# Kernel optimization log

Measured on AMD Instinct MI355X. Metric: run time of the kernel, lower is better.

The kernel has to match this reference:

```python
import jax, jax.numpy as jnp
import numpy as np

# geomloss SamplesLoss('sinkhorn', blur=0.5, scaling=0.9, reach=None) defaults: p=2, debias=True
P = 2
BLUR = 0.5
SCALING = 0.9


def _sqdist_half(a, b):
    # C(x,y) = |x-y|^2 / 2  (geomloss p=2 cost), shape [N, M]
    a2 = jnp.sum(a * a, axis=1)
    b2 = jnp.sum(b * b, axis=1)
    return 0.5 * (a2[:, None] + b2[None, :]) - a @ b.T


def _softmin(eps, C, h):
    # softmin_tensorized: -eps * logsumexp_j( h_j - C_ij / eps ),  h = log-weights + dual/eps
    return -eps * jax.nn.logsumexp(h[None, :] - C / eps, axis=1)


def _eps_schedule(x, y):
    # geomloss epsilon_schedule: anneal eps from diameter^p down to blur^p by scaling^p
    xn, yn = np.asarray(x), np.asarray(y)
    mins = np.minimum(xn.min(axis=0), yn.min(axis=0))
    maxs = np.maximum(xn.max(axis=0), yn.max(axis=0))
    diameter = float(np.linalg.norm(maxs - mins))
    eps_list = [diameter ** P]
    eps_list += [float(np.exp(e)) for e in
                 np.arange(P * np.log(diameter), P * np.log(BLUR), P * np.log(SCALING))]
    eps_list += [BLUR ** P]
    return eps_list


def _sinkhorn_divergence(x, y, eps_list):
    N, M = x.shape[0], y.shape[0]
    C_xy = _sqdist_half(x, y)
    C_yx = C_xy.T
    C_xx = _sqdist_half(x, x)
    C_yy = _sqdist_half(y, y)
    a_log = jnp.full((N,), -float(np.log(N)), dtype=x.dtype)  # uniform weights, log domain
    b_log = jnp.full((M,), -float(np.log(M)), dtype=x.dtype)

    sg = jax.lax.stop_gradient
    Cxy_d, Cyx_d = sg(C_xy), sg(C_yx)
    Cxx_d, Cyy_d = sg(C_xx), sg(C_yy)

    # init at largest eps (= diameter^p)
    eps0 = eps_list[0]
    f_ba = _softmin(eps0, Cxy_d, b_log)
    g_ab = _softmin(eps0, Cyx_d, a_log)
    f_aa = _softmin(eps0, Cxx_d, a_log)
    g_bb = _softmin(eps0, Cyy_d, b_log)

    # symmetric (averaged) Sinkhorn updates along the eps-scaling schedule (no grad, like geomloss)
    for eps in eps_list:
        ft_ba = _softmin(eps, Cxy_d, b_log + g_ab / eps)
        gt_ab = _softmin(eps, Cyx_d, a_log + f_ba / eps)
        ft_aa = _softmin(eps, Cxx_d, a_log + f_aa / eps)
        gt_bb = _softmin(eps, Cyy_d, b_log + g_bb / eps)
        f_ba, g_ab = 0.5 * (f_ba + ft_ba), 0.5 * (g_ab + gt_ab)
        f_aa, g_bb = 0.5 * (f_aa + ft_aa), 0.5 * (g_bb + gt_bb)

    # last extrapolation at eps = blur^p; gradient flows only through the cost matrices here
    eps = eps_list[-1]
    f_ba, g_ab = (_softmin(eps, C_xy, sg(b_log + g_ab / eps)),
                  _softmin(eps, C_yx, sg(a_log + f_ba / eps)))
    f_aa = _softmin(eps, C_xx, sg(a_log + f_aa / eps))
    g_bb = _softmin(eps, C_yy, sg(b_log + g_bb / eps))

    # debiased divergence: <alpha, f_ba - f_aa> + <beta, g_ab - g_bb> (uniform weights -> mean)
    return jnp.mean(f_ba - f_aa) + jnp.mean(g_ab - g_bb)


def setup_inputs() -> dict:
    key = jax.random.key(0)
    kx, ky = jax.random.split(key)
    x = jax.random.normal(kx, (4096, 32), dtype=jnp.float32)
    y = jax.random.normal(ky, (4096, 32), dtype=jnp.float32)
    return {"x": x, "y": y}


def reference(x, y):
    eps_list = _eps_schedule(x, y)  # data-dependent schedule computed eagerly (as geomloss does)
    return _sinkhorn_divergence(x, y, eps_list)
```

## Files before the change

kernel.cpp:

```cpp
#include <hip/hip_runtime.h>
#include <math.h>

#define NPTS 4096
#define DIM  32
#define MAXSLOTS 52
#define NTHREADS 256
#define ITHREADS 512
#define NELEM 131072

#define WS_N2X   0
#define WS_N2Y   4096
#define WS_PMIN  8192
#define WS_PMAX  10240
#define WS_EPS   12288
#define WS_MODE  12352
#define WS_DUAL  12416
#define DUALSZ   16384
#define WS_BF    45184

#define M_SKIP   0
#define M_INIT   1
#define M_AVG    2
#define M_ASSIGN 3

typedef short   short8 __attribute__((ext_vector_type(8)));
typedef _Float16 half8 __attribute__((ext_vector_type(8)));
typedef float   f32x4  __attribute__((ext_vector_type(4)));

__device__ __forceinline__ float exp2fast(float a){
#if __has_builtin(__builtin_amdgcn_exp2f)
    return __builtin_amdgcn_exp2f(a);
#else
    return exp2f(a);
#endif
}
__device__ __forceinline__ float log2fast(float a){
#if __has_builtin(__builtin_amdgcn_logf)
    return __builtin_amdgcn_logf(a);
#else
    return log2f(a);
#endif
}

__global__ void sink_norms(const float* __restrict__ x, const float* __restrict__ y,
                           float* __restrict__ ws)
{
    int row = blockIdx.x * blockDim.x + threadIdx.x;
    const float* src = (row < NPTS) ? (x + (size_t)row * DIM)
                                    : (y + (size_t)(row - NPTS) * DIM);
    const float4* s4 = (const float4*)src;
    float acc = 0.f;
#pragma unroll
    for (int q = 0; q < 8; q++) {
        float4 v = s4[q];
        acc += v.x*v.x + v.y*v.y + v.z*v.z + v.w*v.w;
    }
    ws[row] = 0.5f * acc;
}

__global__ void sink_prep(const float* __restrict__ x, const float* __restrict__ y,
                          unsigned short* __restrict__ bf)
{
    int tid = blockIdx.x * 256 + threadIdx.x;
    int e = tid * 8;
    const float* src = (e < NELEM) ? (x + e) : (y + (e - NELEM));
    float4 v0 = ((const float4*)src)[0];
    float4 v1 = ((const float4*)src)[1];
    float vs[8] = {v0.x, v0.y, v0.z, v0.w, v1.x, v1.y, v1.z, v1.w};
    short hv[8];
#pragma unroll
    for (int i = 0; i < 8; i++) {
        union { _Float16 f; short s; } u;
        u.f = (_Float16)vs[i];
        hv[i] = u.s;
    }
    short8 hvec = {hv[0],hv[1],hv[2],hv[3],hv[4],hv[5],hv[6],hv[7]};
    *(short8*)((short*)bf + e) = hvec;
}

__global__ void sink_minmax(const float* __restrict__ x, const float* __restrict__ y,
                            float* __restrict__ ws)
{
    __shared__ float2 mm[8][32];
    int t = threadIdx.x;
    int d = t & 31, rg = t >> 5;
    float mn = 3.4e38f, mx = -3.4e38f;
#pragma unroll
    for (int k = 0; k < 16; k++) {
        int row = blockIdx.x * 128 + k * 8 + rg;
        const float* src = (row < NPTS) ? (x + (size_t)row * DIM)
                                        : (y + (size_t)(row - NPTS) * DIM);
        float v = src[d];
        mn = fminf(mn, v); mx = fmaxf(mx, v);
    }
    mm[rg][d] = make_float2(mn, mx);
    __syncthreads();
    if (t < 32) {
        float2 a = mm[0][t];
#pragma unroll
        for (int g = 1; g < 8; g++) {
            float2 b = mm[g][t];
            a.x = fminf(a.x, b.x); a.y = fmaxf(a.y, b.y);
        }
        ws[WS_PMIN + blockIdx.x * 32 + t] = a.x;
        ws[WS_PMAX + blockIdx.x * 32 + t] = a.y;
    }
}

__global__ void sink_sched(float* __restrict__ ws)
{
    __shared__ float mins[32], maxs[32];
    int t = threadIdx.x;
    if (t < 32) {
        float mn = 3.4e38f, mx = -3.4e38f;
        for (int b = 0; b < 64; b++) {
            mn = fminf(mn, ws[WS_PMIN + b * 32 + t]);
            mx = fmaxf(mx, ws[WS_PMAX + b * 32 + t]);
        }
        mins[t] = mn; maxs[t] = mx;
    }
    __syncthreads();
    if (t == 0) {
        float dia2 = 0.f;
        for (int d = 0; d < 32; d++) {
            float df = maxs[d] - mins[d];
            dia2 += df * df;
        }
        float dia = sqrtf(dia2);
        float* eps = ws + WS_EPS;
        int*  mode = (int*)(ws + WS_MODE);
        double ld    = log((double)dia);
        double start = 2.0 * ld;
        double stop  = 2.0 * log(0.5);
        double step  = 2.0 * log(0.9);
        int K = (int)ceil((stop - start) / step);
        if (K < 0) K = 0;
        if (K > MAXSLOTS - 5) K = MAXSLOTS - 5;
        eps[0] = dia * dia; mode[0] = M_INIT;
        eps[1] = dia * dia; mode[1] = M_AVG;
        for (int k = 0; k < K; k++) {
            eps[2 + k] = (float)exp(start + step * (double)k);
            mode[2 + k] = M_AVG;
        }
        eps[2 + K] = 0.25f; mode[2 + K] = M_AVG;
        eps[3 + K] = 0.25f; mode[3 + K] = M_ASSIGN;
        for (int s = 4 + K; s < MAXSLOTS; s++) { eps[s] = 0.25f; mode[s] = M_SKIP; }
    }
}

#define GLSE(T, R) \
    { float v0 = fmaf(ca##T[0][R], ie2, hpr[0]); \
      float v1 = fmaf(ca##T[1][R], ie2, hpr[1]); \
      float v2 = fmaf(ca##T[2][R], ie2, hpr[2]); \
      float v3 = fmaf(ca##T[3][R], ie2, hpr[3]); \
      float gm = fmaxf(fmaxf(v0, v1), v2); \
      float nm = fmaxf(fmaxf(gm, v3), ms##T[R]); \
      float er = exp2fast(ms##T[R] - nm); \
      float e0 = exp2fast(v0 - nm); \
      float e1 = exp2fast(v1 - nm); \
      float e2 = exp2fast(v2 - nm); \
      float e3 = exp2fast(v3 - nm); \
      ss##T[R] = fmaf(ss##T[R], er, (e0 + e1) + (e2 + e3)); \
      ms##T[R] = nm; }

__global__ __launch_bounds__(ITHREADS, 4) void sink_iter(float* __restrict__ ws, int slot)
{
    const int t = threadIdx.x;
    const int mode = ((const int*)(ws + WS_MODE))[slot];

    if (mode == M_SKIP) {
        int idx = blockIdx.x * ITHREADS + t;
        if (idx < DUALSZ)
            ws[WS_DUAL + ((slot + 1) & 1) * DUALSZ + idx] =
                ws[WS_DUAL + (slot & 1) * DUALSZ + idx];
        return;
    }

    const float eps     = ws[WS_EPS + slot];
    const float inv_eps = 1.0f / eps;
    const float L2E     = 1.4426950408889634f;
    const float LN2     = 0.6931471805599453f;
    const float ie2     = inv_eps * L2E;
    const float hbase   = -8.317766166719343f;
    const float don     = (mode == M_INIT) ? 0.0f : 1.0f;

    const int bm   = blockIdx.x >> 7;
    const int tile = blockIdx.x & 127;
    const int S    = (blockIdx.x * 5) & 31;
    const int rowIsX = (bm == 0 || bm == 2);
    const int colIsX = (bm == 1 || bm == 2);

    const short* bf = (const short*)(ws + WS_BF);
    const short* rbase = bf + (rowIsX ? 0 : NELEM);
    const short* cbase = bf + (colIsX ? 0 : NELEM);
    const float* rn2 = ws + (rowIsX ? WS_N2X : WS_N2Y);
    const float* cn2 = ws + (colIsX ? WS_N2X : WS_N2Y);

    const float* bufold = ws + WS_DUAL + (slot & 1) * DUALSZ;
    float*       bufnew = ws + WS_DUAL + ((slot + 1) & 1) * DUALSZ;
    const int dualsel = (bm == 0) ? 1 : (bm == 1) ? 0 : bm;
    const float* dual   = bufold + dualsel * NPTS;
    const float* oldout = bufold + bm * NPTS;
    float*       out    = bufnew + bm * NPTS;

    __shared__ float  hps[NPTS];
    __shared__ float2 parts[8][32];

    const int lane = t & 63;
    const int wv   = t >> 6;
    const int lr   = lane & 15;
    const int lk   = (lane >> 4) * 8;

    const int ar0 = tile * 32 + lr;
    const half8 a0 = *(const half8*)(rbase + ar0 * DIM + lk);
    const half8 a1 = *(const half8*)(rbase + (ar0 + 16) * DIM + lk);

    const int colbase = wv * 512;
    const short* cwb = cbase + (size_t)colbase * DIM;
    const int laneoff = lr * DIM + lk;

    half8 bh[3];
#pragma unroll
    for (int p = 0; p < 3; p++) {
        const int w0 = ((p + S) & 31) * (16 * DIM);
        bh[p] = *(const half8*)(cwb + w0 + laneoff);
    }

#pragma unroll
    for (int q = 0; q < 8; q++) {
        int j = t + q * ITHREADS;
        hps[j] = (hbase + fmaf(don, dual[j], -cn2[j]) * inv_eps) * L2E;
    }
    __syncthreads();

    float ms0[4] = {-INFINITY, -INFINITY, -INFINITY, -INFINITY};
    float ms1[4] = {-INFINITY, -INFINITY, -INFINITY, -INFINITY};
    float ss0[4] = {0.f, 0.f, 0.f, 0.f};
    float ss1[4] = {0.f, 0.f, 0.f, 0.f};

    f32x4 ca0[4], ca1[4];
    float hpr[4];

#pragma unroll
    for (int ct = 0; ct < 32; ct++) {
        const half8 hB = bh[ct % 3];
        f32x4 u0 = {0.f, 0.f, 0.f, 0.f};
        f32x4 u1 = {0.f, 0.f, 0.f, 0.f};
        u0 = __builtin_amdgcn_mfma_f32_16x16x32_f16(a0, hB, u0, 0, 0, 0);
        u1 = __builtin_amdgcn_mfma_f32_16x16x32_f16(a1, hB, u1, 0, 0, 0);
        if (ct < 29) {
            const int wn = (((ct + 3) + S) & 31) * (16 * DIM);
            bh[ct % 3] = *(const half8*)(cwb + wn + laneoff);
        }
        const int wc = ((ct + S) & 31) * 16;
        hpr[ct & 3] = hps[colbase + wc + lr];
        ca0[ct & 3] = u0;
        ca1[ct & 3] = u1;
        if ((ct & 3) == 3) {
            GLSE(0, 0) GLSE(0, 1) GLSE(0, 2) GLSE(0, 3)
            GLSE(1, 0) GLSE(1, 1) GLSE(1, 2) GLSE(1, 3)
        }
    }

#pragma unroll
    for (int wm = 1; wm <= 8; wm <<= 1) {
#pragma unroll
        for (int r = 0; r < 4; r++) {
            float om, os, nm;
            om = __shfl_xor(ms0[r], wm, 64); os = __shfl_xor(ss0[r], wm, 64);
            nm = fmaxf(ms0[r], om);
            ss0[r] = fmaf(ss0[r], exp2fast(ms0[r] - nm), os * exp2fast(om - nm));
            ms0[r] = nm;
            om = __shfl_xor(ms1[r], wm, 64); os = __shfl_xor(ss1[r], wm, 64);
            nm = fmaxf(ms1[r], om);
            ss1[r] = fmaf(ss1[r], exp2fast(ms1[r] - nm), os * exp2fast(om - nm));
            ms1[r] = nm;
        }
    }
    if (lr == 0) {
        const int g4 = (lane >> 4) * 4;
#pragma unroll
        for (int r = 0; r < 4; r++) {
            parts[wv][g4 + r]      = make_float2(ms0[r], ss0[r]);
            parts[wv][16 + g4 + r] = make_float2(ms1[r], ss1[r]);
        }
    }
    __syncthreads();
    if (t < 32) {
        float2 p = parts[0][t];
        float m = p.x, s = p.y;
#pragma unroll
        for (int w2 = 1; w2 < 8; w2++) {
            float2 q = parts[w2][t];
            float nm = fmaxf(m, q.x);
            s = fmaf(s, exp2fast(m - nm), q.y * exp2fast(q.x - nm));
            m = nm;
        }
        const float lse = LN2 * (m + log2fast(s));
        const int row = tile * 32 + t;
        const float ft = rn2[row] - eps * lse;
        out[row] = (mode == M_AVG) ? 0.5f * (oldout[row] + ft) : ft;
    }
}

__global__ void sink_reduce(const float* __restrict__ ws, float* __restrict__ outp)
{
    __shared__ float red[NTHREADS];
    const float* b = ws + WS_DUAL;
    int t = threadIdx.x;
    float acc = 0.f;
    for (int i = t; i < NPTS; i += NTHREADS)
        acc += (b[i] - b[2 * NPTS + i]) + (b[NPTS + i] - b[3 * NPTS + i]);
    red[t] = acc;
    __syncthreads();
    for (int s = NTHREADS / 2; s > 0; s >>= 1) {
        if (t < s) red[t] += red[t + s];
        __syncthreads();
    }
    if (t == 0) outp[0] = red[0] * (1.0f / (float)NPTS);
}

extern "C" void kernel_launch(void* const* d_in, const int* in_sizes, int n_in,
                              void* d_out, int out_size, void* d_ws, size_t ws_size,
                              hipStream_t stream)
{
    const float* x = (const float*)d_in[0];
    const float* y = (const float*)d_in[1];
    float* ws  = (float*)d_ws;
    float* out = (float*)d_out;

    hipLaunchKernelGGL(sink_norms,  dim3(32),  dim3(NTHREADS), 0, stream, x, y, ws);
    hipLaunchKernelGGL(sink_prep,   dim3(128), dim3(NTHREADS), 0, stream, x, y,
                       (unsigned short*)(ws + WS_BF));
    hipLaunchKernelGGL(sink_minmax, dim3(64),  dim3(NTHREADS), 0, stream, x, y, ws);
    hipLaunchKernelGGL(sink_sched,  dim3(1),   dim3(NTHREADS), 0, stream, ws);
    for (int s = 0; s < MAXSLOTS; s++)
        hipLaunchKernelGGL(sink_iter, dim3(512), dim3(ITHREADS), 0, stream, ws, s);
    hipLaunchKernelGGL(sink_reduce, dim3(1), dim3(NTHREADS), 0, stream, ws, out);
}
```

Before: 901.7 us.

## Split row tiles across waves and skip rescaling when running max is unchanged

Each wave now handles one 16-row half-tile over a 1024-column window instead of both halves over 512 columns. This halves the accumulator registers and allows a higher launch-bounds occupancy hint. The online logsumexp skips recomputing the rescale exponential when no lane's new max exceeds the running max, using a wave-wide vote. The hps values are prefetched into registers together with the B fragments, and the eps-schedule slot cap is lowered from 52 to 50, which risks truncating long schedules.

```diff
diff --git a/kernel.cpp b/kernel.cpp
--- a/kernel.cpp
+++ b/kernel.cpp
@@ -3,7 +3,7 @@
 
 #define NPTS 4096
 #define DIM  32
-#define MAXSLOTS 52
+#define MAXSLOTS 50
 #define NTHREADS 256
 #define ITHREADS 512
 #define NELEM 131072
@@ -148,22 +148,7 @@
     }
 }
 
-#define GLSE(T, R) \
-    { float v0 = fmaf(ca##T[0][R], ie2, hpr[0]); \
-      float v1 = fmaf(ca##T[1][R], ie2, hpr[1]); \
-      float v2 = fmaf(ca##T[2][R], ie2, hpr[2]); \
-      float v3 = fmaf(ca##T[3][R], ie2, hpr[3]); \
-      float gm = fmaxf(fmaxf(v0, v1), v2); \
-      float nm = fmaxf(fmaxf(gm, v3), ms##T[R]); \
-      float er = exp2fast(ms##T[R] - nm); \
-      float e0 = exp2fast(v0 - nm); \
-      float e1 = exp2fast(v1 - nm); \
-      float e2 = exp2fast(v2 - nm); \
-      float e3 = exp2fast(v3 - nm); \
-      ss##T[R] = fmaf(ss##T[R], er, (e0 + e1) + (e2 + e3)); \
-      ms##T[R] = nm; }
-
-__global__ __launch_bounds__(ITHREADS, 4) void sink_iter(float* __restrict__ ws, int slot)
+__global__ __launch_bounds__(ITHREADS, 6) void sink_iter(float* __restrict__ ws, int slot)
 {
     const int t = threadIdx.x;
     const int mode = ((const int*)(ws + WS_MODE))[slot];
@@ -186,7 +171,7 @@
 
     const int bm   = blockIdx.x >> 7;
     const int tile = blockIdx.x & 127;
-    const int S    = (blockIdx.x * 5) & 31;
+    const int S    = (blockIdx.x * 11) & 63;
     const int rowIsX = (bm == 0 || bm == 2);
     const int colIsX = (bm == 1 || bm == 2);
 
@@ -204,27 +189,18 @@
     float*       out    = bufnew + bm * NPTS;
 
     __shared__ float  hps[NPTS];
-    __shared__ float2 parts[8][32];
+    __shared__ float2 parts[8][16];
 
     const int lane = t & 63;
     const int wv   = t >> 6;
     const int lr   = lane & 15;
     const int lk   = (lane >> 4) * 8;
 
-    const int ar0 = tile * 32 + lr;
-    const half8 a0 = *(const half8*)(rbase + ar0 * DIM + lk);
-    const half8 a1 = *(const half8*)(rbase + (ar0 + 16) * DIM + lk);
-
-    const int colbase = wv * 512;
-    const short* cwb = cbase + (size_t)colbase * DIM;
-    const int laneoff = lr * DIM + lk;
-
-    half8 bh[3];
-#pragma unroll
-    for (int p = 0; p < 3; p++) {
-        const int w0 = ((p + S) & 31) * (16 * DIM);
-        bh[p] = *(const half8*)(cwb + w0 + laneoff);
-    }
+    const int tsel = wv >> 2;
+    const int cwin = (wv & 3) << 10;
+
+    const int ar = tile * 32 + tsel * 16 + lr;
+    const half8 a0 = *(const half8*)(rbase + ar * DIM + lk);
 
 #pragma unroll
     for (int q = 0; q < 8; q++) {
@@ -233,32 +209,54 @@
     }
     __syncthreads();
 
-    float ms0[4] = {-INFINITY, -INFINITY, -INFINITY, -INFINITY};
-    float ms1[4] = {-INFINITY, -INFINITY, -INFINITY, -INFINITY};
-    float ss0[4] = {0.f, 0.f, 0.f, 0.f};
-    float ss1[4] = {0.f, 0.f, 0.f, 0.f};
-
-    f32x4 ca0[4], ca1[4];
+    const short* cwb = cbase + (size_t)cwin * DIM;
+    const int laneoff = lr * DIM + lk;
+    const float* hpw = hps + cwin + lr;
+
+    half8 bh[4];
+    float hpv[4];
+#pragma unroll
+    for (int p = 0; p < 4; p++) {
+        const int w = (p + S) & 63;
+        bh[p]  = *(const half8*)(cwb + w * (16 * DIM) + laneoff);
+        hpv[p] = hpw[w * 16];
+    }
+
+    float ms[4] = {-INFINITY, -INFINITY, -INFINITY, -INFINITY};
+    float ss[4] = {0.f, 0.f, 0.f, 0.f};
+    f32x4 ca[4];
     float hpr[4];
 
-#pragma unroll
-    for (int ct = 0; ct < 32; ct++) {
-        const half8 hB = bh[ct % 3];
-        f32x4 u0 = {0.f, 0.f, 0.f, 0.f};
-        f32x4 u1 = {0.f, 0.f, 0.f, 0.f};
-        u0 = __builtin_amdgcn_mfma_f32_16x16x32_f16(a0, hB, u0, 0, 0, 0);
-        u1 = __builtin_amdgcn_mfma_f32_16x16x32_f16(a1, hB, u1, 0, 0, 0);
-        if (ct < 29) {
-            const int wn = (((ct + 3) + S) & 31) * (16 * DIM);
-            bh[ct % 3] = *(const half8*)(cwb + wn + laneoff);
-        }
-        const int wc = ((ct + S) & 31) * 16;
-        hpr[ct & 3] = hps[colbase + wc + lr];
-        ca0[ct & 3] = u0;
-        ca1[ct & 3] = u1;
-        if ((ct & 3) == 3) {
-            GLSE(0, 0) GLSE(0, 1) GLSE(0, 2) GLSE(0, 3)
-            GLSE(1, 0) GLSE(1, 1) GLSE(1, 2) GLSE(1, 3)
+    for (int g = 0; g < 16; g++) {
+#pragma unroll
+        for (int sl = 0; sl < 4; sl++) {
+            const int ct = g * 4 + sl;
+            const half8 hB = bh[sl];
+            f32x4 u = {0.f, 0.f, 0.f, 0.f};
+            u = __builtin_amdgcn_mfma_f32_16x16x32_f16(a0, hB, u, 0, 0, 0);
+            hpr[sl] = hpv[sl];
+            const int w = ((ct + 4) + S) & 63;
+            bh[sl]  = *(const half8*)(cwb + w * (16 * DIM) + laneoff);
+            hpv[sl] = hpw[w * 16];
+            ca[sl] = u;
+        }
+#pragma unroll
+        for (int r = 0; r < 4; r++) {
+            const float v0 = fmaf(ca[0][r], ie2, hpr[0]);
+            const float v1 = fmaf(ca[1][r], ie2, hpr[1]);
+            const float v2 = fmaf(ca[2][r], ie2, hpr[2]);
+            const float v3 = fmaf(ca[3][r], ie2, hpr[3]);
+            const float gm = fmaxf(fmaxf(v0, v1), fmaxf(v2, v3));
+            if (__any(gm > ms[r])) {
+                const float nm = fmaxf(ms[r], gm);
+                ss[r] = fmaf(ss[r], exp2fast(ms[r] - nm),
+                             (exp2fast(v0 - nm) + exp2fast(v1 - nm)) +
+                             (exp2fast(v2 - nm) + exp2fast(v3 - nm)));
+                ms[r] = nm;
+            } else {
+                ss[r] += (exp2fast(v0 - ms[r]) + exp2fast(v1 - ms[r])) +
+                         (exp2fast(v2 - ms[r]) + exp2fast(v3 - ms[r]));
+            }
         }
     }
 
@@ -266,32 +264,28 @@
     for (int wm = 1; wm <= 8; wm <<= 1) {
 #pragma unroll
         for (int r = 0; r < 4; r++) {
-            float om, os, nm;
-            om = __shfl_xor(ms0[r], wm, 64); os = __shfl_xor(ss0[r], wm, 64);
-            nm = fmaxf(ms0[r], om);
-            ss0[r] = fmaf(ss0[r], exp2fast(ms0[r] - nm), os * exp2fast(om - nm));
-            ms0[r] = nm;
-            om = __shfl_xor(ms1[r], wm, 64); os = __shfl_xor(ss1[r], wm, 64);
-            nm = fmaxf(ms1[r], om);
-            ss1[r] = fmaf(ss1[r], exp2fast(ms1[r] - nm), os * exp2fast(om - nm));
-            ms1[r] = nm;
+            float om = __shfl_xor(ms[r], wm, 64);
+            float os = __shfl_xor(ss[r], wm, 64);
+            float nm = fmaxf(ms[r], om);
+            ss[r] = fmaf(ss[r], exp2fast(ms[r] - nm), os * exp2fast(om - nm));
+            ms[r] = nm;
         }
     }
     if (lr == 0) {
         const int g4 = (lane >> 4) * 4;
 #pragma unroll
-        for (int r = 0; r < 4; r++) {
-            parts[wv][g4 + r]      = make_float2(ms0[r], ss0[r]);
-            parts[wv][16 + g4 + r] = make_float2(ms1[r], ss1[r]);
-        }
+        for (int r = 0; r < 4; r++)
+            parts[wv][g4 + r] = make_float2(ms[r], ss[r]);
     }
     __syncthreads();
     if (t < 32) {
-        float2 p = parts[0][t];
+        const int half = t >> 4;
+        const int rr   = t & 15;
+        float2 p = parts[half * 4][rr];
         float m = p.x, s = p.y;
 #pragma unroll
-        for (int w2 = 1; w2 < 8; w2++) {
-            float2 q = parts[w2][t];
+        for (int w2 = 1; w2 < 4; w2++) {
+            float2 q = parts[half * 4 + w2][rr];
             float nm = fmaxf(m, q.x);
             s = fmaf(s, exp2fast(m - nm), q.y * exp2fast(q.x - nm));
             m = nm;
```

New measurement: 993.4 us. 1.1x slower.
